# Kernel tuning notes

Measured on AMD Instinct MI355X. Metric: run time of the kernel, lower is better.

## Reference

```python
import jax, jax.numpy as jnp
import numpy as np

N_NODES = 100000
N_EDGES = 640000
D_FEAT = 128
HIDDEN = 128
FINAL = 64
N_GRAPHS = 128


def setup_inputs() -> dict:
    key = jax.random.key(0)
    ks = jax.random.split(key, 8)
    x = jax.random.normal(ks[0], (N_NODES, D_FEAT), dtype=jnp.float32)
    edge_index = jax.random.randint(ks[1], (2, N_EDGES), 0, N_NODES, dtype=jnp.int64)
    batch = jnp.sort(jax.random.randint(ks[2], (N_NODES,), 0, N_GRAPHS, dtype=jnp.int64))
    # SAGEConv params: lin_l (aggregated neighbors, with bias), lin_r (self, no bias)
    W_l = jax.random.normal(ks[3], (HIDDEN, D_FEAT), dtype=jnp.float32) / np.sqrt(D_FEAT)
    b_l = jnp.zeros((HIDDEN,), dtype=jnp.float32)
    W_r = jax.random.normal(ks[4], (HIDDEN, D_FEAT), dtype=jnp.float32) / np.sqrt(D_FEAT)
    # Final linear head on column_stack([max_pool, mean_pool])
    W_lin = jax.random.normal(ks[5], (FINAL, 2 * HIDDEN), dtype=jnp.float32) / np.sqrt(2 * HIDDEN)
    b_lin = jnp.zeros((FINAL,), dtype=jnp.float32)
    return {"x": x, "edge_index": edge_index, "batch": batch,
            "W_l": W_l, "b_l": b_l, "W_r": W_r, "W_lin": W_lin, "b_lin": b_lin}


def reference(x, edge_index, batch, W_l, b_l, W_r, W_lin, b_lin):
    N = x.shape[0]
    src, dst = edge_index[0], edge_index[1]
    # SAGEConv: mean-aggregate neighbor messages src -> dst
    agg = jax.ops.segment_sum(x[src], dst, num_segments=N)  # [N, D]
    deg = jax.ops.segment_sum(jnp.ones_like(src, dtype=x.dtype), dst, num_segments=N)
    agg = agg / jnp.maximum(deg, 1.0)[:, None]
    h = agg @ W_l.T + b_l + x @ W_r.T  # [N, HIDDEN]
    h = jax.nn.relu(h)
    # global max / mean pool over graphs in batch
    x_max = jax.ops.segment_max(h, batch, num_segments=N_GRAPHS)  # [G, HIDDEN]
    cnt = jax.ops.segment_sum(jnp.ones((N,), h.dtype), batch, num_segments=N_GRAPHS)
    x_mean = jax.ops.segment_sum(h, batch, num_segments=N_GRAPHS) / jnp.maximum(cnt, 1.0)[:, None]
    z = jnp.concatenate([x_max, x_mean], axis=1)  # [G, 2*HIDDEN]
    # dropout is identity in eval mode (training=False)
    return z @ W_lin.T + b_lin
```

## Files before the change

### kernel.cpp

```cpp
#include <hip/hip_runtime.h>
#include <math.h>

#define NN 100000
#define NE 640000
#define NG 128
#define NF 64
#define MAXDEG 32

typedef __attribute__((ext_vector_type(8))) short short8;
typedef __attribute__((ext_vector_type(4))) float floatx4;

__device__ __forceinline__ unsigned short bf16_rne(float v) {
    unsigned u = __float_as_uint(v);
    return (unsigned short)((u + 0x7FFF + ((u >> 16) & 1)) >> 16);
}
__device__ __forceinline__ void split2(float f0, float f1, unsigned& H, unsigned& L) {
    unsigned short h0 = bf16_rne(f0), h1 = bf16_rne(f1);
    float r0 = f0 - __uint_as_float((unsigned)h0 << 16);
    float r1 = f1 - __uint_as_float((unsigned)h1 << 16);
    H = (unsigned)h0 | ((unsigned)h1 << 16);
    L = (unsigned)bf16_rne(r0) | ((unsigned)bf16_rne(r1) << 16);
}

__global__ __launch_bounds__(256) void k_bucket(const int* __restrict__ ei,
                                                int* __restrict__ cnt,
                                                int* __restrict__ slot) {
    int e = blockIdx.x * 256 + threadIdx.x;
    if (e >= NE) return;
    int src = ei[e];
    int dst = ei[NE + e];
    int pos = atomicAdd(&cnt[dst], 1);
    if (pos < MAXDEG) slot[dst * MAXDEG + pos] = src;
}

__global__ __launch_bounds__(256) void k_prepW(const float* __restrict__ Wl,
                                               const float* __restrict__ Wr,
                                               unsigned short* __restrict__ Bhi,
                                               unsigned short* __restrict__ Blo) {
    int idx = blockIdx.x * 256 + threadIdx.x;
    if (idx >= 256 * 128) return;
    int k = idx >> 7;
    int j = idx & 127;
    float v = (k < 128) ? Wl[j * 128 + k] : Wr[j * 128 + (k - 128)];
    int c = k >> 5, nb = j >> 4;
    int l = (j & 15) + (((k >> 3) & 3) << 4);
    int e = k & 7;
    int off = ((c * 8 + nb) * 64 + l) * 8 + e;
    unsigned short hb = bf16_rne(v);
    float hf = __uint_as_float((unsigned)hb << 16);
    Bhi[off] = hb;
    Blo[off] = bf16_rne(v - hf);
}

__global__ __launch_bounds__(256) void k_fused(const float* __restrict__ x,
                                               const int* __restrict__ slot,
                                               const int* __restrict__ cnt,
                                               const int* __restrict__ batch,
                                               const unsigned short* __restrict__ Bhi,
                                               const unsigned short* __restrict__ Blo,
                                               const float* __restrict__ bl,
                                               float* __restrict__ pmax,
                                               float* __restrict__ psum) {
    __shared__ unsigned short Ahi_s[2 * 8 * 64 * 8];
    __shared__ unsigned short Alo_s[2 * 8 * 64 * 8];
    __shared__ int sbatch[32];
    int tid = threadIdx.x;
    int wave = tid >> 6, lane = tid & 63;
    int g = lane >> 4, i = lane & 15;
    int n0 = blockIdx.x * 32;
    if (tid < 32) sbatch[tid] = batch[n0 + tid];

    const float4* x4 = (const float4*)x;
    for (int p = 0; p < 2; ++p) {
        int ln = wave * 8 + p * 4 + g;
        int n = n0 + ln;
        int ctrue = cnt[n];
        float inv = 1.f / fmaxf((float)ctrue, 1.f);
        int c = ctrue > MAXDEG ? MAXDEG : ctrue;
        int idx0 = slot[n * MAXDEG + i];
        int idx1 = slot[n * MAXDEG + 16 + i];
        int cmax = c;
        cmax = max(cmax, __shfl_xor(cmax, 16));
        cmax = max(cmax, __shfl_xor(cmax, 32));
        float4 a0 = make_float4(0.f, 0.f, 0.f, 0.f);
        float4 a1 = make_float4(0.f, 0.f, 0.f, 0.f);
        for (int e = 0; e < cmax; ++e) {
            int s = (e < 16) ? __shfl(idx0, (lane & 48) + e)
                             : __shfl(idx1, (lane & 48) + (e - 16));
            if (e < c) {
                float4 v0 = x4[(size_t)s * 32 + 2 * i];
                float4 v1 = x4[(size_t)s * 32 + 2 * i + 1];
                a0.x += v0.x; a0.y += v0.y; a0.z += v0.z; a0.w += v0.w;
                a1.x += v1.x; a1.y += v1.y; a1.z += v1.z; a1.w += v1.w;
            }
        }
        a0.x *= inv; a0.y *= inv; a0.z *= inv; a0.w *= inv;
        a1.x *= inv; a1.y *= inv; a1.z *= inv; a1.w *= inv;
        int base = (((ln >> 4) * 8 + (i >> 2)) * 64 + (ln & 15) + ((i & 3) << 4)) * 8;
        uint4 H, L;
        split2(a0.x, a0.y, H.x, L.x);
        split2(a0.z, a0.w, H.y, L.y);
        split2(a1.x, a1.y, H.z, L.z);
        split2(a1.z, a1.w, H.w, L.w);
        *(uint4*)&Ahi_s[base] = H;
        *(uint4*)&Alo_s[base] = L;
        float4 s0 = x4[(size_t)n * 32 + 2 * i];
        float4 s1 = x4[(size_t)n * 32 + 2 * i + 1];
        split2(s0.x, s0.y, H.x, L.x);
        split2(s0.z, s0.w, H.y, L.y);
        split2(s1.x, s1.y, H.z, L.z);
        split2(s1.z, s1.w, H.w, L.w);
        *(uint4*)&Ahi_s[base + 4 * 64 * 8] = H;
        *(uint4*)&Alo_s[base + 4 * 64 * 8] = L;
    }
    __syncthreads();

    int wm = wave >> 1, wn = wave & 1;
    floatx4 acc[4];
    #pragma unroll
    for (int n = 0; n < 4; ++n) acc[n] = (floatx4){0.f, 0.f, 0.f, 0.f};
    #pragma unroll
    for (int c = 0; c < 8; ++c) {
        short8 ah = *(const short8*)&Ahi_s[((wm * 8 + c) * 64 + lane) * 8];
        short8 al = *(const short8*)&Alo_s[((wm * 8 + c) * 64 + lane) * 8];
        #pragma unroll
        for (int n = 0; n < 4; ++n) {
            int nb = wn * 4 + n;
            int off = ((c * 8 + nb) * 64 + lane) * 8;
            short8 bh = *(const short8*)&Bhi[off];
            short8 bo = *(const short8*)&Blo[off];
            acc[n] = __builtin_amdgcn_mfma_f32_16x16x32_bf16(ah, bh, acc[n], 0, 0, 0);
            acc[n] = __builtin_amdgcn_mfma_f32_16x16x32_bf16(ah, bo, acc[n], 0, 0, 0);
            acc[n] = __builtin_amdgcn_mfma_f32_16x16x32_bf16(al, bh, acc[n], 0, 0, 0);
        }
    }

    int colb = wn * 64 + i;
    float v[4][4];
    #pragma unroll
    for (int n = 0; n < 4; ++n) {
        float bv = bl[colb + n * 16];
        #pragma unroll
        for (int r = 0; r < 4; ++r) v[n][r] = fmaxf(acc[n][r] + bv, 0.f);
    }
    int myg[4];
    #pragma unroll
    for (int r = 0; r < 4; ++r) myg[r] = sbatch[wm * 16 + g * 4 + r];
    int gfirst = sbatch[wm * 16];
    int glast  = sbatch[wm * 16 + 15];
    for (int gg = gfirst; gg <= glast; ++gg) {
        #pragma unroll
        for (int n = 0; n < 4; ++n) {
            float mx = 0.f, sm = 0.f;
            #pragma unroll
            for (int r = 0; r < 4; ++r) {
                if (myg[r] == gg) { mx = fmaxf(mx, v[n][r]); sm += v[n][r]; }
            }
            mx = fmaxf(mx, __shfl_xor(mx, 16));
            mx = fmaxf(mx, __shfl_xor(mx, 32));
            sm += __shfl_xor(sm, 16);
            sm += __shfl_xor(sm, 32);
            if (lane < 16) {
                atomicMax((unsigned*)&pmax[gg * 128 + colb + n * 16], __float_as_uint(mx));
                atomicAdd(&psum[gg * 128 + colb + n * 16], sm);
            }
        }
    }
}

__global__ __launch_bounds__(128) void k_pool2head(const float* __restrict__ pmax,
                                                   const float* __restrict__ psum,
                                                   const int* __restrict__ batch,
                                                   const float* __restrict__ Wlin,
                                                   const float* __restrict__ blin,
                                                   float* __restrict__ out) {
    int g = blockIdx.x;
    int t = threadIdx.x;
    int lo = 0, hi = NN;
    while (lo < hi) { int mid = (lo + hi) >> 1; if (batch[mid] < g) lo = mid + 1; else hi = mid; }
    int start = lo;
    hi = NN;
    while (lo < hi) { int mid = (lo + hi) >> 1; if (batch[mid] < g + 1) lo = mid + 1; else hi = mid; }
    int cntg = lo - start;
    __shared__ float z[256];
    z[t]       = pmax[g * 128 + t];
    z[128 + t] = psum[g * 128 + t] / fmaxf((float)cntg, 1.f);
    __syncthreads();
    if (t < 64) {
        float acc = blin[t];
        const float* w = &Wlin[t * 256];
        #pragma unroll 8
        for (int c = 0; c < 256; ++c) acc = fmaf(z[c], w[c], acc);
        out[g * 64 + t] = acc;
    }
}

extern "C" void kernel_launch(void* const* d_in, const int* in_sizes, int n_in,
                              void* d_out, int out_size, void* d_ws, size_t ws_size,
                              hipStream_t stream) {
    const float* x     = (const float*)d_in[0];
    const int*   ei    = (const int*)d_in[1];
    const int*   batch = (const int*)d_in[2];
    const float* Wl    = (const float*)d_in[3];
    const float* bl    = (const float*)d_in[4];
    const float* Wr    = (const float*)d_in[5];
    const float* Wlin  = (const float*)d_in[6];
    const float* blin  = (const float*)d_in[7];
    float* out = (float*)d_out;

    char* ws = (char*)d_ws;
    int*   cnt  = (int*)(ws);
    int*   slot = (int*)(ws + 409600);
    float* pmax = (float*)(ws + 13209600);
    float* psum = (float*)(ws + 13275136);
    unsigned short* Bhi = (unsigned short*)(ws + 13340672);
    unsigned short* Blo = (unsigned short*)(ws + 13406208);

    hipMemsetAsync(cnt, 0, NN * sizeof(int), stream);
    hipMemsetAsync(pmax, 0, NG * 128 * sizeof(float), stream);
    hipMemsetAsync(psum, 0, NG * 128 * sizeof(float), stream);
    k_prepW<<<128, 256, 0, stream>>>(Wl, Wr, Bhi, Blo);
    k_bucket<<<NE / 256, 256, 0, stream>>>(ei, cnt, slot);
    k_fused<<<NN / 32, 256, 0, stream>>>(x, slot, cnt, batch, Bhi, Blo, bl, pmax, psum);
    k_pool2head<<<NG, 128, 0, stream>>>(pmax, psum, batch, Wlin, blin, out);
}
```

Before: 229.9 us.

## Halve fused-kernel LDS by splitting GEMM into two K-phases; merge prep launches

The fused kernel now stages only half of the A operand in shared memory at a time: it runs the aggregated-neighbour half of the K reduction, then reuses the same buffer for the self-feature half. This halves LDS per block, and launch bounds of 8 blocks per multiprocessor are added to raise occupancy. The extra barriers and the serialised phases can cost some latency hiding. Separately, the three memsets become one zeroing kernel and the weight-prep and bucketing kernels are merged into one launch, cutting launch overhead.

```diff
diff --git a/kernel.cpp b/kernel.cpp
--- a/kernel.cpp
+++ b/kernel.cpp
@@ -22,47 +22,54 @@
     L = (unsigned)bf16_rne(r0) | ((unsigned)bf16_rne(r1) << 16);
 }
 
-__global__ __launch_bounds__(256) void k_bucket(const int* __restrict__ ei,
-                                                int* __restrict__ cnt,
-                                                int* __restrict__ slot) {
-    int e = blockIdx.x * 256 + threadIdx.x;
-    if (e >= NE) return;
-    int src = ei[e];
-    int dst = ei[NE + e];
-    int pos = atomicAdd(&cnt[dst], 1);
-    if (pos < MAXDEG) slot[dst * MAXDEG + pos] = src;
-}
-
-__global__ __launch_bounds__(256) void k_prepW(const float* __restrict__ Wl,
-                                               const float* __restrict__ Wr,
-                                               unsigned short* __restrict__ Bhi,
-                                               unsigned short* __restrict__ Blo) {
+__global__ __launch_bounds__(256) void k_zero(int* __restrict__ cnt,
+                                              float* __restrict__ pools) {
     int idx = blockIdx.x * 256 + threadIdx.x;
-    if (idx >= 256 * 128) return;
-    int k = idx >> 7;
-    int j = idx & 127;
-    float v = (k < 128) ? Wl[j * 128 + k] : Wr[j * 128 + (k - 128)];
-    int c = k >> 5, nb = j >> 4;
-    int l = (j & 15) + (((k >> 3) & 3) << 4);
-    int e = k & 7;
-    int off = ((c * 8 + nb) * 64 + l) * 8 + e;
-    unsigned short hb = bf16_rne(v);
-    float hf = __uint_as_float((unsigned)hb << 16);
-    Bhi[off] = hb;
-    Blo[off] = bf16_rne(v - hf);
-}
-
-__global__ __launch_bounds__(256) void k_fused(const float* __restrict__ x,
-                                               const int* __restrict__ slot,
-                                               const int* __restrict__ cnt,
-                                               const int* __restrict__ batch,
-                                               const unsigned short* __restrict__ Bhi,
-                                               const unsigned short* __restrict__ Blo,
-                                               const float* __restrict__ bl,
-                                               float* __restrict__ pmax,
-                                               float* __restrict__ psum) {
-    __shared__ unsigned short Ahi_s[2 * 8 * 64 * 8];
-    __shared__ unsigned short Alo_s[2 * 8 * 64 * 8];
+    if (idx < NN) cnt[idx] = 0;
+    else if (idx < NN + 2 * NG * 128) pools[idx - NN] = 0.f;
+}
+
+__global__ __launch_bounds__(256) void k_prep(const int* __restrict__ ei,
+                                              int* __restrict__ cnt,
+                                              int* __restrict__ slot,
+                                              const float* __restrict__ Wl,
+                                              const float* __restrict__ Wr,
+                                              unsigned short* __restrict__ Bhi,
+                                              unsigned short* __restrict__ Blo) {
+    if (blockIdx.x < 128) {
+        int idx = blockIdx.x * 256 + threadIdx.x;
+        int k = idx >> 7;
+        int j = idx & 127;
+        float v = (k < 128) ? Wl[j * 128 + k] : Wr[j * 128 + (k - 128)];
+        int c = k >> 5, nb = j >> 4;
+        int l = (j & 15) + (((k >> 3) & 3) << 4);
+        int e = k & 7;
+        int off = ((c * 8 + nb) * 64 + l) * 8 + e;
+        unsigned short hb = bf16_rne(v);
+        float hf = __uint_as_float((unsigned)hb << 16);
+        Bhi[off] = hb;
+        Blo[off] = bf16_rne(v - hf);
+    } else {
+        int e = (blockIdx.x - 128) * 256 + threadIdx.x;
+        if (e >= NE) return;
+        int src = ei[e];
+        int dst = ei[NE + e];
+        int pos = atomicAdd(&cnt[dst], 1);
+        if (pos < MAXDEG) slot[dst * MAXDEG + pos] = src;
+    }
+}
+
+__global__ __launch_bounds__(256, 8) void k_fused(const float* __restrict__ x,
+                                                  const int* __restrict__ slot,
+                                                  const int* __restrict__ cnt,
+                                                  const int* __restrict__ batch,
+                                                  const unsigned short* __restrict__ Bhi,
+                                                  const unsigned short* __restrict__ Blo,
+                                                  const float* __restrict__ bl,
+                                                  float* __restrict__ pmax,
+                                                  float* __restrict__ psum) {
+    __shared__ unsigned short Ahi_s[2 * 4 * 64 * 8];
+    __shared__ unsigned short Alo_s[2 * 4 * 64 * 8];
     __shared__ int sbatch[32];
     int tid = threadIdx.x;
     int wave = tid >> 6, lane = tid & 63;
@@ -71,6 +78,11 @@
     if (tid < 32) sbatch[tid] = batch[n0 + tid];
 
     const float4* x4 = (const float4*)x;
+    int wm = wave >> 1, wn = wave & 1;
+    floatx4 acc[4];
+    #pragma unroll
+    for (int n = 0; n < 4; ++n) acc[n] = (floatx4){0.f, 0.f, 0.f, 0.f};
+
     for (int p = 0; p < 2; ++p) {
         int ln = wave * 8 + p * 4 + g;
         int n = n0 + ln;
@@ -96,7 +108,7 @@
         }
         a0.x *= inv; a0.y *= inv; a0.z *= inv; a0.w *= inv;
         a1.x *= inv; a1.y *= inv; a1.z *= inv; a1.w *= inv;
-        int base = (((ln >> 4) * 8 + (i >> 2)) * 64 + (ln & 15) + ((i & 3) << 4)) * 8;
+        int base = (((ln >> 4) * 4 + (i >> 2)) * 64 + (ln & 15) + ((i & 3) << 4)) * 8;
         uint4 H, L;
         split2(a0.x, a0.y, H.x, L.x);
         split2(a0.z, a0.w, H.y, L.y);
@@ -104,29 +116,48 @@
         split2(a1.z, a1.w, H.w, L.w);
         *(uint4*)&Ahi_s[base] = H;
         *(uint4*)&Alo_s[base] = L;
+    }
+    __syncthreads();
+    #pragma unroll
+    for (int c = 0; c < 4; ++c) {
+        short8 ah = *(const short8*)&Ahi_s[((wm * 4 + c) * 64 + lane) * 8];
+        short8 al = *(const short8*)&Alo_s[((wm * 4 + c) * 64 + lane) * 8];
+        #pragma unroll
+        for (int n = 0; n < 4; ++n) {
+            int nb = wn * 4 + n;
+            int off = ((c * 8 + nb) * 64 + lane) * 8;
+            short8 bh = *(const short8*)&Bhi[off];
+            short8 bo = *(const short8*)&Blo[off];
+            acc[n] = __builtin_amdgcn_mfma_f32_16x16x32_bf16(ah, bh, acc[n], 0, 0, 0);
+            acc[n] = __builtin_amdgcn_mfma_f32_16x16x32_bf16(ah, bo, acc[n], 0, 0, 0);
+            acc[n] = __builtin_amdgcn_mfma_f32_16x16x32_bf16(al, bh, acc[n], 0, 0, 0);
+        }
+    }
+    __syncthreads();
+
+    for (int p = 0; p < 2; ++p) {
+        int ln = wave * 8 + p * 4 + g;
+        int n = n0 + ln;
         float4 s0 = x4[(size_t)n * 32 + 2 * i];
         float4 s1 = x4[(size_t)n * 32 + 2 * i + 1];
+        int base = (((ln >> 4) * 4 + (i >> 2)) * 64 + (ln & 15) + ((i & 3) << 4)) * 8;
+        uint4 H, L;
         split2(s0.x, s0.y, H.x, L.x);
         split2(s0.z, s0.w, H.y, L.y);
         split2(s1.x, s1.y, H.z, L.z);
         split2(s1.z, s1.w, H.w, L.w);
-        *(uint4*)&Ahi_s[base + 4 * 64 * 8] = H;
-        *(uint4*)&Alo_s[base + 4 * 64 * 8] = L;
-    }
-    __syncthreads();
-
-    int wm = wave >> 1, wn = wave & 1;
-    floatx4 acc[4];
-    #pragma unroll
-    for (int n = 0; n < 4; ++n) acc[n] = (floatx4){0.f, 0.f, 0.f, 0.f};
-    #pragma unroll
-    for (int c = 0; c < 8; ++c) {
-        short8 ah = *(const short8*)&Ahi_s[((wm * 8 + c) * 64 + lane) * 8];
-        short8 al = *(const short8*)&Alo_s[((wm * 8 + c) * 64 + lane) * 8];
+        *(uint4*)&Ahi_s[base] = H;
+        *(uint4*)&Alo_s[base] = L;
+    }
+    __syncthreads();
+    #pragma unroll
+    for (int c = 0; c < 4; ++c) {
+        short8 ah = *(const short8*)&Ahi_s[((wm * 4 + c) * 64 + lane) * 8];
+        short8 al = *(const short8*)&Alo_s[((wm * 4 + c) * 64 + lane) * 8];
         #pragma unroll
         for (int n = 0; n < 4; ++n) {
             int nb = wn * 4 + n;
-            int off = ((c * 8 + nb) * 64 + lane) * 8;
+            int off = (((c + 4) * 8 + nb) * 64 + lane) * 8;
             short8 bh = *(const short8*)&Bhi[off];
             short8 bo = *(const short8*)&Blo[off];
             acc[n] = __builtin_amdgcn_mfma_f32_16x16x32_bf16(ah, bh, acc[n], 0, 0, 0);
@@ -216,11 +247,8 @@
     unsigned short* Bhi = (unsigned short*)(ws + 13340672);
     unsigned short* Blo = (unsigned short*)(ws + 13406208);
 
-    hipMemsetAsync(cnt, 0, NN * sizeof(int), stream);
-    hipMemsetAsync(pmax, 0, NG * 128 * sizeof(float), stream);
-    hipMemsetAsync(psum, 0, NG * 128 * sizeof(float), stream);
-    k_prepW<<<128, 256, 0, stream>>>(Wl, Wr, Bhi, Blo);
-    k_bucket<<<NE / 256, 256, 0, stream>>>(ei, cnt, slot);
+    k_zero<<<(NN + 2 * NG * 128 + 255) / 256, 256, 0, stream>>>(cnt, pmax);
+    k_prep<<<128 + (NE + 255) / 256, 256, 0, stream>>>(ei, cnt, slot, Wl, Wr, Bhi, Blo);
     k_fused<<<NN / 32, 256, 0, stream>>>(x, slot, cnt, batch, Bhi, Blo, bl, pmax, psum);
     k_pool2head<<<NG, 128, 0, stream>>>(pmax, psum, batch, Wlin, blin, out);
 }
```

Result: faster. 211.6 us (-8.0%).
